# Kernel optimization log

Hardware: AMD Instinct MI355X
Metric: run time of the kernel (lower is better)

## Reference

```python
import jax, jax.numpy as jnp
import numpy as np

B, T, M, P = 256, 128, 64, 64


def setup_inputs() -> dict:
    key = jax.random.key(0)
    ks = jax.random.split(key, 20)
    s = 0.05
    inp = {
        "data": jax.random.normal(ks[0], (B, T - 1, 1), jnp.float32),
        "encoder_h": jax.random.normal(ks[1], (B, T, M), jnp.float32),
        "h0": jax.random.normal(ks[2], (B, P), jnp.float32),
        "s0": jax.random.normal(ks[3], (B, P), jnp.float32),
        # dense: Dense(1) on concat([x, context]) -> in=1+M
        "W_dense": jax.random.normal(ks[4], (1 + M, 1), jnp.float32) * s,
        "b_dense": jnp.zeros((1,), jnp.float32),
        # LSTM(p): kernel (1,4p), recurrent (p,4p), bias (4p); keras gate order i,f,c,o
        "Wk": jax.random.normal(ks[5], (1, 4 * P), jnp.float32) * s,
        "Uk": jax.random.normal(ks[6], (P, 4 * P), jnp.float32) * s,
        "bk": jnp.zeros((4 * P,), jnp.float32),
        # temporal attention: W_d Dense(m) on concat([h,c]) (2p -> m)
        "Wd": jax.random.normal(ks[7], (2 * P, M), jnp.float32) * s,
        "bWd": jnp.zeros((M,), jnp.float32),
        # U_d Dense(m) on encoder_h (m -> m)
        "Ud": jax.random.normal(ks[8], (M, M), jnp.float32) * s,
        "bUd": jnp.zeros((M,), jnp.float32),
        # v_d Dense(1)
        "vd": jax.random.normal(ks[9], (M, 1), jnp.float32) * s,
        "bvd": jnp.zeros((1,), jnp.float32),
        # dense_vb: Dense(1) on concat([h, context]) (p+m -> 1)
        "Wvb": jax.random.normal(ks[10], (P + M, 1), jnp.float32) * s,
        "bvb": jnp.zeros((1,), jnp.float32),
        # dense_Wb: Dense(p) applied AFTER dense_vb (1 -> p), as in the source
        "Wb": jax.random.normal(ks[11], (1, P), jnp.float32) * s,
        "bWb": jnp.zeros((P,), jnp.float32),
    }
    return inp


def reference(data, encoder_h, h0, s0, W_dense, b_dense, Wk, Uk, bk,
              Wd, bWd, Ud, bUd, vd, bvd, Wvb, bvb, Wb, bWb):
    # Loop-invariant: U_d(encoder_h), (B,T,M). Math identical to per-step compute.
    Ue = jnp.einsum('btm,mn->btn', encoder_h, Ud) + bUd

    def step(carry, x_t):
        ctx, _h = carry                      # ctx: (B,M)
        inp = jnp.concatenate([x_t, ctx], axis=-1)   # (B, 1+M)
        y = inp @ W_dense + b_dense                   # (B,1)
        # NOTE: source resets LSTM state to (h0, s0) at every step.
        z = y @ Wk + h0 @ Uk + bk                     # (B,4P)
        i_g, f_g, g_g, o_g = jnp.split(z, 4, axis=-1)
        c = jax.nn.sigmoid(f_g) * s0 + jax.nn.sigmoid(i_g) * jnp.tanh(g_g)
        h = jax.nn.sigmoid(o_g) * jnp.tanh(c)         # (B,P)
        # temporal attention
        dproj = jnp.concatenate([h, c], axis=-1) @ Wd + bWd   # (B,M)
        e = jnp.tanh(dproj[:, None, :] + Ue) @ vd + bvd        # (B,T,1)
        beta = jax.nn.softmax(e, axis=1)                       # (B,T,1)
        ctx_new = jnp.einsum('bti,btm->bm', beta, encoder_h)   # (B,M)
        return (ctx_new, h), None

    Bsz = encoder_h.shape[0]
    carry0 = (jnp.zeros((Bsz, Wk.shape[1] // 4 * 0 + encoder_h.shape[2]), encoder_h.dtype),
              jnp.zeros((Bsz, Uk.shape[0]), encoder_h.dtype))
    xs = jnp.transpose(data, (1, 0, 2))  # (T-1, B, 1)
    (ctx, h), _ = jax.lax.scan(step, carry0, xs)

    concatenated = jnp.concatenate([h, ctx], axis=-1)[:, None, :]  # (B,1,P+M)
    out = (concatenated @ Wvb + bvb) @ Wb + bWb                     # (B,1,P)
    return out
```

## Files before the change

kernel.cpp:

```cpp
#include <hip/hip_runtime.h>


#define Bn 256
#define Tn 128
#define Mn 64
#define Pn 64
#define NTH 512
#define NW 8
#define UST 68
#define DPST 72
#define K2C 2.885390081777927f

typedef float f32x2 __attribute__((ext_vector_type(2)));

__device__ __forceinline__ float fexp(float x) {
    return __builtin_amdgcn_exp2f(x * 1.44269504088896341f);
}
__device__ __forceinline__ float fexp2(float x) { return __builtin_amdgcn_exp2f(x); }
__device__ __forceinline__ float frcp(float x) { return __builtin_amdgcn_rcpf(x); }
__device__ __forceinline__ float fsig(float x) { return frcp(1.0f + fexp(-x)); }
__device__ __forceinline__ float ftanh(float x) { return 1.0f - 2.0f * frcp(1.0f + fexp(2.0f * x)); }

template <int CTRL>
__device__ __forceinline__ float dppmov(float x) {
    return __int_as_float(__builtin_amdgcn_update_dpp(
        0, __float_as_int(x), CTRL, 0xf, 0xf, false));
}
__device__ __forceinline__ float rdlane(float x, int l) {
    return __int_as_float(__builtin_amdgcn_readlane(__float_as_int(x), l));
}
__device__ __forceinline__ float wavesum63(float x) {
    x += dppmov<0x111>(x);
    x += dppmov<0x112>(x);
    x += dppmov<0x114>(x);
    x += dppmov<0x118>(x);
    x += dppmov<0x142>(x);
    x += dppmov<0x143>(x);
    return x;
}

#define OFF_ENC   0
#define OFF_UD    8704
#define OFF_PRE   13056
#define OFF_DPART 13312
#define OFF_DPW   13888
#define OFF_YSDEN 14464
#define OFF_CTXP  14496
#define SMEM_FLOATS 15008

__global__ __launch_bounds__(NTH, 2)
void decoder_kernel(const float* __restrict__ data, const float* __restrict__ enc,
                    const float* __restrict__ h0, const float* __restrict__ s0,
                    const float* __restrict__ W_dense, const float* __restrict__ b_dense,
                    const float* __restrict__ Wk, const float* __restrict__ Uk,
                    const float* __restrict__ bk,
                    const float* __restrict__ Wd, const float* __restrict__ bWd,
                    const float* __restrict__ Ud, const float* __restrict__ bUd,
                    const float* __restrict__ vd, const float* __restrict__ bvd,
                    const float* __restrict__ Wvb, const float* __restrict__ bvb,
                    const float* __restrict__ Wb, const float* __restrict__ bWb,
                    float* __restrict__ out)
{
    extern __shared__ float smem[];
    float* enc_s  = smem + OFF_ENC;
    float* Ud_s   = smem + OFF_UD;
    float* pre_s  = smem + OFF_PRE;
    float* dpart  = smem + OFF_DPART;
    float* dprojw = smem + OFF_DPW;
    f32x2* ysden  = (f32x2*)(smem + OFF_YSDEN);
    float* ctxp   = smem + OFF_CTXP;

    const int b    = blockIdx.x;
    const int tid  = threadIdx.x;
    const int lane = tid & 63;
    const int wv   = tid >> 6;

    {
        const float* encg = enc + (size_t)b * Tn * Mn;
        #pragma unroll
        for (int i = 0; i < 4; i++) {
            int flat = (i * NTH + tid) * 4;
            int t = flat >> 6, m = flat & 63;
            *(float4*)(enc_s + t * UST + m) = *(const float4*)(encg + flat);
        }
        #pragma unroll
        for (int i = 0; i < 2; i++) {
            int flat = (i * NTH + tid) * 4;
            int k = flat >> 6, n = flat & 63;
            *(float4*)(Ud_s + k * UST + n) = *(const float4*)(Ud + flat);
        }
        if (tid < 4 * Pn) {
            float s = bk[tid];
            const float* h0b = h0 + b * Pn;
            #pragma unroll
            for (int k = 0; k < Pn; k++) s = fmaf(h0b[k], Uk[k * 4 * Pn + tid], s);
            pre_s[tid] = s;
        }
        if (tid < 2 * NW) {
            f32x2 z; z.x = 0.0f; z.y = 0.125f;
            ysden[tid] = z;
        }
    }
    __syncthreads();

    const int t_e = 16 * wv + (lane >> 2), q_e = lane & 3, m0 = q_e * 16;
    f32x2 ue2[8];
    {
        float acc[16];
        #pragma unroll
        for (int j = 0; j < 16; j++) acc[j] = bUd[m0 + j];
        for (int k = 0; k < Mn; k++) {
            float a = enc_s[t_e * UST + k];
            const float4* ud = (const float4*)(Ud_s + k * UST + m0);
            #pragma unroll
            for (int j4 = 0; j4 < 4; j4++) {
                float4 u = ud[j4];
                acc[4 * j4 + 0] = fmaf(a, u.x, acc[4 * j4 + 0]);
                acc[4 * j4 + 1] = fmaf(a, u.y, acc[4 * j4 + 1]);
                acc[4 * j4 + 2] = fmaf(a, u.z, acc[4 * j4 + 2]);
                acc[4 * j4 + 3] = fmaf(a, u.w, acc[4 * j4 + 3]);
            }
        }
        #pragma unroll
        for (int j = 0; j < 8; j++) {
            ue2[j].x = K2C * acc[2 * j];
            ue2[j].y = K2C * acc[2 * j + 1];
        }
    }

    float enc_r[16];
    #pragma unroll
    for (int j = 0; j < 16; j++)
        enc_r[j] = enc_s[(16 * wv + j) * UST + lane];
    float wd_r[16];
    #pragma unroll
    for (int j = 0; j < 16; j++)
        wd_r[j] = K2C * Wd[(16 * wv + j) * Mn + lane];
    const float W0  = W_dense[0];
    const float bd  = b_dense[0];
    const float Wde = W_dense[1 + lane];
    const float wk_i = Wk[lane], wk_f = Wk[64 + lane],
                wk_g = Wk[128 + lane], wk_o = Wk[192 + lane];
    const float s0v   = s0[b * Pn + lane];
    const float bvd0  = bvd[0];
    const float bwd_l = K2C * bWd[lane];
    f32x2 vd2[8];
    float sumvd16 = 0.0f;
    #pragma unroll
    for (int j = 0; j < 8; j++) {
        float va = vd[m0 + 2 * j], vb = vd[m0 + 2 * j + 1];
        vd2[j].x = -2.0f * va; vd2[j].y = -2.0f * vb;
        sumvd16 += va + vb;
    }
    const float pre_i = pre_s[lane];
    const float pre_f = pre_s[64 + lane];
    const float pre_g = pre_s[128 + lane];
    const float pre_o = pre_s[192 + lane];
    const bool hv_sel = (wv < 4);
    const int  base16 = (wv & 3) * 16;
    const float* xb = data + (size_t)b * (Tn - 1);
    const float x_lo = xb[lane];
    const float x_hi = (lane < 63) ? xb[64 + lane] : 0.0f;

    float h = 0.0f, c = 0.0f;
    float* dp_my = dprojw + wv * DPST;

    for (int st = 0; st < Tn - 1; ++st) {
        const int par = st & 1, nxt = par ^ 1;

        f32x2 yv = ysden[par * NW + (lane & 7)];
        yv.x += dppmov<0x111>(yv.x); yv.y += dppmov<0x111>(yv.y);
        yv.x += dppmov<0x112>(yv.x); yv.y += dppmov<0x112>(yv.y);
        yv.x += dppmov<0x114>(yv.x); yv.y += dppmov<0x114>(yv.y);
        float ytot = rdlane(yv.x, 7);
        float dtot = rdlane(yv.y, 7);
        float xs = (st < 64) ? rdlane(x_lo, st) : rdlane(x_hi, st - 64);
        float y = fmaf(xs, W0, fmaf(ytot, frcp(dtot), bd));

        float zi = fmaf(y, wk_i, pre_i);
        float zf = fmaf(y, wk_f, pre_f);
        float zg = fmaf(y, wk_g, pre_g);
        float zo = fmaf(y, wk_o, pre_o);
        c = fsig(zf) * s0v + fsig(zi) * ftanh(zg);
        h = fsig(zo) * ftanh(c);

        {
            float hv = hv_sel ? h : c;
            float p0 = 0.0f, p1 = 0.0f, p2 = 0.0f, p3 = 0.0f;
            #pragma unroll
            for (int j = 0; j < 4; j++) {
                p0 = fmaf(rdlane(hv, base16 + j),      wd_r[j],      p0);
                p1 = fmaf(rdlane(hv, base16 + 4 + j),  wd_r[4 + j],  p1);
                p2 = fmaf(rdlane(hv, base16 + 8 + j),  wd_r[8 + j],  p2);
                p3 = fmaf(rdlane(hv, base16 + 12 + j), wd_r[12 + j], p3);
            }
            dpart[wv * DPST + lane] = (p0 + p1) + (p2 + p3);
        }
        __syncthreads();

        {
            float v0 = dpart[0 * DPST + lane] + dpart[1 * DPST + lane];
            float v1 = dpart[2 * DPST + lane] + dpart[3 * DPST + lane];
            float v2 = dpart[4 * DPST + lane] + dpart[5 * DPST + lane];
            float v3 = dpart[6 * DPST + lane] + dpart[7 * DPST + lane];
            dp_my[lane] = ((v0 + v1) + (v2 + v3)) + bwd_l;
        }

        float ex;
        {
            float4 d[4];
            const float4* dp4 = (const float4*)(dp_my + m0);
            #pragma unroll
            for (int i = 0; i < 4; i++) d[i] = dp4[i];
            f32x2 accA; accA.x = sumvd16; accA.y = 0.0f;
            f32x2 accB; accB.x = 0.0f;    accB.y = 0.0f;
            #pragma unroll
            for (int i = 0; i < 4; i++) {
                f32x2 sA, rA, sB, rB;
                sA.x = d[i].x + ue2[2 * i].x;     sA.y = d[i].y + ue2[2 * i].y;
                rA.x = frcp(1.0f + fexp2(sA.x));  rA.y = frcp(1.0f + fexp2(sA.y));
                accA += vd2[2 * i] * rA;
                sB.x = d[i].z + ue2[2 * i + 1].x; sB.y = d[i].w + ue2[2 * i + 1].y;
                rB.x = frcp(1.0f + fexp2(sB.x));  rB.y = frcp(1.0f + fexp2(sB.y));
                accB += vd2[2 * i + 1] * rB;
            }
            f32x2 accT = accA + accB;
            float acc = accT.x + accT.y;
            acc += dppmov<0x111>(acc);
            acc += dppmov<0x112>(acc);
            ex = fexp(acc + bvd0);
        }

        {
            float p0 = 0.0f, p1 = 0.0f, p2 = 0.0f, p3 = 0.0f;
            #pragma unroll
            for (int j = 0; j < 4; j++) {
                p0 = fmaf(rdlane(ex, 4 * j + 3),        enc_r[j],      p0);
                p1 = fmaf(rdlane(ex, 4 * (j + 4) + 3),  enc_r[4 + j],  p1);
                p2 = fmaf(rdlane(ex, 4 * (j + 8) + 3),  enc_r[8 + j],  p2);
                p3 = fmaf(rdlane(ex, 4 * (j + 12) + 3), enc_r[12 + j], p3);
            }
            float ctxpart = (p0 + p1) + (p2 + p3);
            if (st == Tn - 2) ctxp[wv * 64 + lane] = ctxpart;
            f32x2 w2;
            w2.x = ctxpart * Wde;
            w2.y = ((lane & 3) == 3) ? ex : 0.0f;
            w2.x += dppmov<0x111>(w2.x); w2.y += dppmov<0x111>(w2.y);
            w2.x += dppmov<0x112>(w2.x); w2.y += dppmov<0x112>(w2.y);
            w2.x += dppmov<0x114>(w2.x); w2.y += dppmov<0x114>(w2.y);
            w2.x += dppmov<0x118>(w2.x); w2.y += dppmov<0x118>(w2.y);
            w2.x += dppmov<0x142>(w2.x); w2.y += dppmov<0x142>(w2.y);
            w2.x += dppmov<0x143>(w2.x); w2.y += dppmov<0x143>(w2.y);
            if (lane == 63) ysden[nxt * NW + wv] = w2;
        }
        __syncthreads();
    }

    if (wv == 0) {
        float dtot = 0.0f;
        #pragma unroll
        for (int w = 0; w < NW; w++) dtot += ysden[NW + w].y;
        float invS = frcp(dtot);
        float ctxm = 0.0f;
        #pragma unroll
        for (int w = 0; w < NW; w++) ctxm += ctxp[w * 64 + lane];
        ctxm *= invS;
        float part = h * Wvb[lane] + ctxm * Wvb[64 + lane];
        float v = rdlane(wavesum63(part), 63) + bvb[0];
        out[(size_t)b * Pn + lane] = fmaf(v, Wb[lane], bWb[lane]);
    }
}

extern "C" void kernel_launch(void* const* d_in, const int* in_sizes, int n_in,
                              void* d_out, int out_size, void* d_ws, size_t ws_size,
                              hipStream_t stream) {
    const float* data    = (const float*)d_in[0];
    const float* enc     = (const float*)d_in[1];
    const float* h0      = (const float*)d_in[2];
    const float* s0      = (const float*)d_in[3];
    const float* W_dense = (const float*)d_in[4];
    const float* b_dense = (const float*)d_in[5];
    const float* Wk      = (const float*)d_in[6];
    const float* Uk      = (const float*)d_in[7];
    const float* bk      = (const float*)d_in[8];
    const float* Wd      = (const float*)d_in[9];
    const float* bWd     = (const float*)d_in[10];
    const float* Ud      = (const float*)d_in[11];
    const float* bUd     = (const float*)d_in[12];
    const float* vd      = (const float*)d_in[13];
    const float* bvd     = (const float*)d_in[14];
    const float* Wvb     = (const float*)d_in[15];
    const float* bvb     = (const float*)d_in[16];
    const float* Wb      = (const float*)d_in[17];
    const float* bWb     = (const float*)d_in[18];

    decoder_kernel<<<Bn, NTH, SMEM_FLOATS * sizeof(float), stream>>>(
        data, enc, h0, s0, W_dense, b_dense, Wk, Uk, bk,
        Wd, bWd, Ud, bUd, vd, bvd, Wvb, bvb, Wb, bWb, (float*)d_out);
}
```

Baseline: 283.7 us.

## Precompute encoder-weight projection and factor exp out of attention tanh

The per-step context vector is only needed through its dot product with W_dense. The loop therefore now uses a precomputed per-timestep scalar (encoder_h·W_dense) times the softmax numerator, and the full context is computed only on the last step. The attention tanh term is rewritten so that exp(Ue) is precomputed once. Each step now needs one exp per dproj element plus an fma-and-rcp per element, instead of an exp per (t,m) pair. This removes the per-step 16-lane broadcast FMA loop and most exp calls. The risk is possible overflow or inf in the product of exponentials for large arguments, which changes numerical behavior.

```diff
diff --git a/kernel.cpp b/kernel.cpp
--- a/kernel.cpp
+++ b/kernel.cpp
@@ -104,7 +104,7 @@
     __syncthreads();
 
     const int t_e = 16 * wv + (lane >> 2), q_e = lane & 3, m0 = q_e * 16;
-    f32x2 ue2[8];
+    f32x2 ue_e2[8];
     {
         float acc[16];
         #pragma unroll
@@ -123,22 +123,17 @@
         }
         #pragma unroll
         for (int j = 0; j < 8; j++) {
-            ue2[j].x = K2C * acc[2 * j];
-            ue2[j].y = K2C * acc[2 * j + 1];
-        }
-    }
-
-    float enc_r[16];
-    #pragma unroll
-    for (int j = 0; j < 16; j++)
-        enc_r[j] = enc_s[(16 * wv + j) * UST + lane];
+            ue_e2[j].x = fexp2(K2C * acc[2 * j]);
+            ue_e2[j].y = fexp2(K2C * acc[2 * j + 1]);
+        }
+    }
+
     float wd_r[16];
     #pragma unroll
     for (int j = 0; j < 16; j++)
         wd_r[j] = K2C * Wd[(16 * wv + j) * Mn + lane];
     const float W0  = W_dense[0];
     const float bd  = b_dense[0];
-    const float Wde = W_dense[1 + lane];
     const float wk_i = Wk[lane], wk_f = Wk[64 + lane],
                 wk_g = Wk[128 + lane], wk_o = Wk[192 + lane];
     const float s0v   = s0[b * Pn + lane];
@@ -152,6 +147,12 @@
         vd2[j].x = -2.0f * va; vd2[j].y = -2.0f * vb;
         sumvd16 += va + vb;
     }
+    float ewt = 0.0f;
+    {
+        const float* er = enc_s + t_e * UST;
+        #pragma unroll
+        for (int m = 0; m < Mn; m++) ewt = fmaf(er[m], W_dense[1 + m], ewt);
+    }
     const float pre_i = pre_s[lane];
     const float pre_f = pre_s[64 + lane];
     const float pre_g = pre_s[128 + lane];
@@ -203,7 +204,7 @@
             float v1 = dpart[2 * DPST + lane] + dpart[3 * DPST + lane];
             float v2 = dpart[4 * DPST + lane] + dpart[5 * DPST + lane];
             float v3 = dpart[6 * DPST + lane] + dpart[7 * DPST + lane];
-            dp_my[lane] = ((v0 + v1) + (v2 + v3)) + bwd_l;
+            dp_my[lane] = fexp2(((v0 + v1) + (v2 + v3)) + bwd_l);
         }
 
         float ex;
@@ -216,12 +217,13 @@
             f32x2 accB; accB.x = 0.0f;    accB.y = 0.0f;
             #pragma unroll
             for (int i = 0; i < 4; i++) {
-                f32x2 sA, rA, sB, rB;
-                sA.x = d[i].x + ue2[2 * i].x;     sA.y = d[i].y + ue2[2 * i].y;
-                rA.x = frcp(1.0f + fexp2(sA.x));  rA.y = frcp(1.0f + fexp2(sA.y));
+                f32x2 eA = ue_e2[2 * i], eB = ue_e2[2 * i + 1];
+                f32x2 rA, rB;
+                rA.x = frcp(fmaf(eA.x, d[i].x, 1.0f));
+                rA.y = frcp(fmaf(eA.y, d[i].y, 1.0f));
                 accA += vd2[2 * i] * rA;
-                sB.x = d[i].z + ue2[2 * i + 1].x; sB.y = d[i].w + ue2[2 * i + 1].y;
-                rB.x = frcp(1.0f + fexp2(sB.x));  rB.y = frcp(1.0f + fexp2(sB.y));
+                rB.x = frcp(fmaf(eB.x, d[i].z, 1.0f));
+                rB.y = frcp(fmaf(eB.y, d[i].w, 1.0f));
                 accB += vd2[2 * i + 1] * rB;
             }
             f32x2 accT = accA + accB;
@@ -232,19 +234,10 @@
         }
 
         {
-            float p0 = 0.0f, p1 = 0.0f, p2 = 0.0f, p3 = 0.0f;
-            #pragma unroll
-            for (int j = 0; j < 4; j++) {
-                p0 = fmaf(rdlane(ex, 4 * j + 3),        enc_r[j],      p0);
-                p1 = fmaf(rdlane(ex, 4 * (j + 4) + 3),  enc_r[4 + j],  p1);
-                p2 = fmaf(rdlane(ex, 4 * (j + 8) + 3),  enc_r[8 + j],  p2);
-                p3 = fmaf(rdlane(ex, 4 * (j + 12) + 3), enc_r[12 + j], p3);
-            }
-            float ctxpart = (p0 + p1) + (p2 + p3);
-            if (st == Tn - 2) ctxp[wv * 64 + lane] = ctxpart;
+            const bool own = ((lane & 3) == 3);
             f32x2 w2;
-            w2.x = ctxpart * Wde;
-            w2.y = ((lane & 3) == 3) ? ex : 0.0f;
+            w2.x = own ? ex * ewt : 0.0f;
+            w2.y = own ? ex : 0.0f;
             w2.x += dppmov<0x111>(w2.x); w2.y += dppmov<0x111>(w2.y);
             w2.x += dppmov<0x112>(w2.x); w2.y += dppmov<0x112>(w2.y);
             w2.x += dppmov<0x114>(w2.x); w2.y += dppmov<0x114>(w2.y);
@@ -252,6 +245,14 @@
             w2.x += dppmov<0x142>(w2.x); w2.y += dppmov<0x142>(w2.y);
             w2.x += dppmov<0x143>(w2.x); w2.y += dppmov<0x143>(w2.y);
             if (lane == 63) ysden[nxt * NW + wv] = w2;
+            if (st == Tn - 2) {
+                float p = 0.0f;
+                #pragma unroll
+                for (int j = 0; j < 16; j++)
+                    p = fmaf(rdlane(ex, 4 * j + 3),
+                             enc_s[(16 * wv + j) * UST + lane], p);
+                ctxp[wv * 64 + lane] = p;
+            }
         }
         __syncthreads();
     }
```

Result: faster. 253.7 us (-10.6%).
